# Kernel tuning notes

Measured on AMD Instinct MI355X. Metric: run time of the kernel, lower is better.

The kernel has to match this reference:

```python
import jax, jax.numpy as jnp
import numpy as np

T, R = 4, 6
HID, HEADS, LAYERS, OUT = 64, 8, 2, 4
DH = HID // HEADS
N = [100000, 200000, 20000, 2000]          # author, paper, term, conference
FEAT = [334, 512, 128, 128]
REL = [(0, 1), (1, 0), (1, 2), (2, 1), (1, 3), (3, 1)]   # (src_type, dst_type)
E = [800000, 800000, 1000000, 1000000, 200000, 200000]
NAMES = ['author', 'paper', 'term', 'conf']


def setup_inputs() -> dict:
    key = jax.random.key(0)
    ks = iter(jax.random.split(key, 64))
    inp = {}
    for t in range(T):
        inp[f'x_{NAMES[t]}'] = jax.random.normal(next(ks), (N[t], FEAT[t]), jnp.float32)
    for t in range(T):
        inp[f'W_in_{NAMES[t]}'] = jax.random.normal(next(ks), (FEAT[t], HID), jnp.float32) / np.sqrt(FEAT[t]).astype(np.float32)
        inp[f'b_in_{NAMES[t]}'] = jnp.zeros((HID,), jnp.float32)
    for nm in ['KW', 'QW', 'VW', 'AW']:
        inp[nm] = jax.random.normal(next(ks), (LAYERS, T, HID, HID), jnp.float32) / np.sqrt(HID).astype(np.float32)
    for nm in ['Kb', 'Qb', 'Vb', 'Ab']:
        inp[nm] = jnp.zeros((LAYERS, T, HID), jnp.float32)
    inp['skip'] = jnp.ones((LAYERS, T), jnp.float32)
    inp['A_rel'] = jax.random.normal(next(ks), (LAYERS, R, HEADS, DH, DH), jnp.float32) / np.sqrt(DH).astype(np.float32)
    inp['M_rel'] = jax.random.normal(next(ks), (LAYERS, R, HEADS, DH, DH), jnp.float32) / np.sqrt(DH).astype(np.float32)
    inp['P_rel'] = jnp.ones((LAYERS, R, HEADS), jnp.float32)
    inp['W_out'] = jax.random.normal(next(ks), (HID, OUT), jnp.float32) / np.sqrt(HID).astype(np.float32)
    inp['b_out'] = jnp.zeros((OUT,), jnp.float32)
    for r in range(R):
        s, d = REL[r]
        src = jax.random.randint(next(ks), (E[r],), 0, N[s], dtype=jnp.int32)
        dst = jax.random.randint(next(ks), (E[r],), 0, N[d], dtype=jnp.int32)
        inp[f'ei_{r}'] = jnp.stack([src, dst])
    return inp


def _segment_softmax(scores, seg, num):
    # scores: [E, HEADS]; softmax over edges sharing the same destination node
    m = jax.ops.segment_max(scores, seg, num_segments=num)
    ex = jnp.exp(scores - m[seg])
    den = jax.ops.segment_sum(ex, seg, num_segments=num)
    return ex / den[seg]


def _forward(xs, Wins, bins, KW, Kb, QW, Qb, VW, Vb, AW, Ab, skip,
             A_rel, M_rel, P_rel, W_out, b_out, eis):
    scale = np.float32(1.0 / np.sqrt(DH))
    h = [jax.nn.relu(x @ W + b) for x, W, b in zip(xs, Wins, bins)]
    for l in range(LAYERS):
        K = [(h[t] @ KW[l, t] + Kb[l, t]).reshape(-1, HEADS, DH) for t in range(T)]
        Q = [(h[t] @ QW[l, t] + Qb[l, t]).reshape(-1, HEADS, DH) for t in range(T)]
        V = [(h[t] @ VW[l, t] + Vb[l, t]).reshape(-1, HEADS, DH) for t in range(T)]
        out = [jnp.zeros((N[t], HID), h[t].dtype) for t in range(T)]
        for r in range(R):
            s, d = REL[r]
            src, dst = eis[r][0], eis[r][1]
            k = jnp.einsum('ehd,hdf->ehf', K[s][src], A_rel[l, r])   # [E,H,dh]
            v = jnp.einsum('ehd,hdf->ehf', V[s][src], M_rel[l, r])
            q = Q[d][dst]
            score = (q * k).sum(-1) * P_rel[l, r] * scale            # [E,H]
            alpha = _segment_softmax(score, dst, N[d])
            msg = (v * alpha[..., None]).reshape(-1, HID)
            out[d] = out[d] + jax.ops.segment_sum(msg, dst, num_segments=N[d])
        newh = []
        for t in range(T):
            o = jax.nn.gelu(out[t], approximate=False) @ AW[l, t] + Ab[l, t]
            g = jax.nn.sigmoid(skip[l, t])
            newh.append(g * o + (1.0 - g) * h[t])
        h = newh
    return h[0] @ W_out + b_out  # author logits


def reference(x_author, x_paper, x_term, x_conf,
              W_in_author, b_in_author, W_in_paper, b_in_paper,
              W_in_term, b_in_term, W_in_conf, b_in_conf,
              KW, Kb, QW, Qb, VW, Vb, AW, Ab, skip,
              A_rel, M_rel, P_rel, W_out, b_out,
              ei_0, ei_1, ei_2, ei_3, ei_4, ei_5):
    xs = [x_author, x_paper, x_term, x_conf]
    Wins = [W_in_author, W_in_paper, W_in_term, W_in_conf]
    bins = [b_in_author, b_in_paper, b_in_term, b_in_conf]
    eis = [ei_0, ei_1, ei_2, ei_3, ei_4, ei_5]
    return _forward(xs, Wins, bins, KW, Kb, QW, Qb, VW, Vb, AW, Ab, skip,
                    A_rel, M_rel, P_rel, W_out, b_out, eis)
```

## Files before the change

kernel.cpp:

```cpp
#include <hip/hip_runtime.h>
#include <math.h>

#define HID 64
#define HEADS 8
#define DH 8
#define TT 4
#define RR 6
#define LAYERS 2
#define NTOT 322000

static const int NS[TT]    = {100000, 200000, 20000, 2000};
static const int FEATS[TT] = {334, 512, 128, 128};
static const int RSRC[RR]  = {0, 1, 1, 2, 1, 3};
static const int RDST[RR]  = {1, 0, 2, 1, 3, 1};


__global__ void fill_f(float* __restrict__ p, float v, int n) {
    int i = blockIdx.x * 256 + threadIdx.x;
    if (i < n) p[i] = v;
}

__global__ void fill_i(int* __restrict__ p, int v, int n) {
    int i = blockIdx.x * 256 + threadIdx.x;
    if (i < n) p[i] = v;
}


__device__ __forceinline__ void load_x16(const float* __restrict__ xp, int F, int k0,
                                         bool f4ok, float xv[16]) {
    int rem = F - k0;
    if (xp && rem > 0) {
        if (rem >= 16) {
            if (f4ok) {
#pragma unroll
                for (int j = 0; j < 4; ++j) {
                    float4 v = *(const float4*)(xp + k0 + 4 * j);
                    xv[4 * j + 0] = v.x; xv[4 * j + 1] = v.y;
                    xv[4 * j + 2] = v.z; xv[4 * j + 3] = v.w;
                }
            } else {
#pragma unroll
                for (int j = 0; j < 8; ++j) {
                    float2 v = *(const float2*)(xp + k0 + 2 * j);
                    xv[2 * j + 0] = v.x; xv[2 * j + 1] = v.y;
                }
            }
        } else {
#pragma unroll
            for (int k = 0; k < 16; ++k) xv[k] = (k < rem) ? xp[k0 + k] : 0.f;
        }
    } else {
#pragma unroll
        for (int k = 0; k < 16; ++k) xv[k] = 0.f;
    }
}

__device__ __forceinline__ float4 load_w4(const float* __restrict__ W, int F,
                                          int f, int c) {
    float4 wv;
    if (f < F) wv = *(const float4*)(W + (size_t)f * 64 + c);
    else { wv.x = 0.f; wv.y = 0.f; wv.z = 0.f; wv.w = 0.f; }
    return wv;
}

template<int PREG, int POST>
__global__ __launch_bounds__(256) void gemm_n64(
    const float* __restrict__ X,
    const float* __restrict__ Wa, const float* __restrict__ Wb, const float* __restrict__ Wc,
    const float* __restrict__ ba, const float* __restrict__ bb, const float* __restrict__ bc,
    float* __restrict__ Ca, float* __restrict__ Cb, float* __restrict__ Cc,
    const float* __restrict__ skipv, int lt,
    int Nrows, int F)
{
    const float* W = Wa; const float* bias = ba; float* C = Ca;
    if (blockIdx.y == 1) { W = Wb; bias = bb; C = Cb; }
    else if (blockIdx.y == 2) { W = Wc; bias = bc; C = Cc; }

    __shared__ float xs[16][256];
    __shared__ float ws[16][64];

    int tid = threadIdx.x;
    int row0 = blockIdx.x * 256;
    int myrow = row0 + tid;
    const float* xp = (myrow < Nrows) ? (X + (size_t)myrow * F) : (const float*)0;

    int cg = tid & 7;
    int rs = tid >> 3;
    int xoff = rs * 8;
    int woff = cg * 8;

    int wi_f = tid >> 4;
    int wi_c = (tid & 15) * 4;

    float acc[8][8];
#pragma unroll
    for (int i = 0; i < 8; ++i)
#pragma unroll
        for (int j = 0; j < 8; ++j) acc[i][j] = 0.f;

    const bool f4ok = ((F & 3) == 0);

    float xv[16];
    float4 wv;
    load_x16(xp, F, 0, f4ok, xv);
    wv = load_w4(W, F, wi_f, wi_c);

    for (int k0 = 0; k0 < F; k0 += 16) {
        __syncthreads();
        if (PREG) {
#pragma unroll
            for (int k = 0; k < 16; ++k) {
                float v = xv[k];
                xs[k][tid] = 0.5f * v * (1.f + erff(v * 0.7071067811865475f));
            }
        } else {
#pragma unroll
            for (int k = 0; k < 16; ++k) xs[k][tid] = xv[k];
        }
        *(float4*)&ws[wi_f][wi_c] = wv;
        __syncthreads();

        if (k0 + 16 < F) {
            load_x16(xp, F, k0 + 16, f4ok, xv);
            wv = load_w4(W, F, k0 + 16 + wi_f, wi_c);
        }

#pragma unroll
        for (int k = 0; k < 16; ++k) {
            float xr[8], wr[8];
#pragma unroll
            for (int j = 0; j < 8; ++j) xr[j] = xs[k][xoff + j];
#pragma unroll
            for (int j = 0; j < 8; ++j) wr[j] = ws[k][woff + j];
#pragma unroll
            for (int i = 0; i < 8; ++i)
#pragma unroll
                for (int j = 0; j < 8; ++j)
                    acc[i][j] = fmaf(xr[i], wr[j], acc[i][j]);
        }
    }

    float bv[8];
#pragma unroll
    for (int j = 0; j < 8; ++j) bv[j] = bias[woff + j];
    float g = 1.f, invg = 0.f;
    if (POST == 2) {
        float s = skipv[lt];
        g = 1.f / (1.f + __expf(-s));
        invg = 1.f - g;
    }
#pragma unroll
    for (int i = 0; i < 8; ++i) {
        int r = row0 + xoff + i;
        if (r < Nrows) {
            size_t base = (size_t)r * 64 + woff;
            float o[8];
#pragma unroll
            for (int j = 0; j < 8; ++j) o[j] = acc[i][j] + bv[j];
            if (POST == 1) {
#pragma unroll
                for (int j = 0; j < 8; ++j) o[j] = fmaxf(o[j], 0.f);
            }
            if (POST == 2) {
#pragma unroll
                for (int j = 0; j < 8; ++j) o[j] = g * o[j] + invg * C[base + j];
            }
            float4 s0, s1;
            s0.x = o[0]; s0.y = o[1]; s0.z = o[2]; s0.w = o[3];
            s1.x = o[4]; s1.y = o[5]; s1.z = o[6]; s1.w = o[7];
            *(float4*)(C + base)     = s0;
            *(float4*)(C + base + 4) = s1;
        }
    }
}

__global__ void out_proj(const float* __restrict__ h, const float* __restrict__ W,
                         const float* __restrict__ b, float* __restrict__ out, int n4) {
    int idx = blockIdx.x * 256 + threadIdx.x;
    if (idx >= n4) return;
    int row = idx >> 2, c = idx & 3;
    float acc = b[c];
    const float* hp = h + (size_t)row * 64;
    for (int f = 0; f < 64; ++f) acc = fmaf(hp[f], W[f * 4 + c], acc);
    out[idx] = acc;
}


__global__ void hist_k(const int* __restrict__ dst, int* __restrict__ deg, int E) {
    int i = blockIdx.x * 256 + threadIdx.x;
    if (i < E) atomicAdd(&deg[dst[i]], 1);
}

__global__ void scan1(const int* __restrict__ deg, int* __restrict__ bsum, int n) {
    __shared__ int sdata[256];
    int tid = threadIdx.x;
    int base = blockIdx.x * 1024 + tid * 4;
    int s = 0;
#pragma unroll
    for (int j = 0; j < 4; ++j) if (base + j < n) s += deg[base + j];
    sdata[tid] = s;
    __syncthreads();
    for (int off = 128; off > 0; off >>= 1) {
        if (tid < off) sdata[tid] += sdata[tid + off];
        __syncthreads();
    }
    if (tid == 0) bsum[blockIdx.x] = sdata[0];
}

__global__ void scan2(int* __restrict__ bsum, int nb) {
    if (blockIdx.x == 0 && threadIdx.x == 0) {
        int run = 0;
        for (int i = 0; i < nb; ++i) { int t = bsum[i]; bsum[i] = run; run += t; }
    }
}

__global__ void scan3(const int* __restrict__ deg, const int* __restrict__ bsum,
                      int* __restrict__ rp, int n, int E) {
    __shared__ int sc[256];
    int tid = threadIdx.x;
    int base = blockIdx.x * 1024 + tid * 4;
    int v0 = 0, v1 = 0, v2 = 0, v3 = 0;
    if (base + 0 < n) v0 = deg[base + 0];
    if (base + 1 < n) v1 = deg[base + 1];
    if (base + 2 < n) v2 = deg[base + 2];
    if (base + 3 < n) v3 = deg[base + 3];
    int s = v0 + v1 + v2 + v3;
    sc[tid] = s;
    __syncthreads();
    for (int off = 1; off < 256; off <<= 1) {
        int t = (tid >= off) ? sc[tid - off] : 0;
        __syncthreads();
        sc[tid] += t;
        __syncthreads();
    }
    int run = bsum[blockIdx.x] + sc[tid] - s;
    if (base + 0 < n) { rp[base + 0] = run; run += v0; }
    if (base + 1 < n) { rp[base + 1] = run; run += v1; }
    if (base + 2 < n) { rp[base + 2] = run; run += v2; }
    if (base + 3 < n) { rp[base + 3] = run; run += v3; }
    if (blockIdx.x == 0 && tid == 0) rp[n] = E;
}

__global__ void scatter_k(const int* __restrict__ src, const int* __restrict__ dst,
                          const int* __restrict__ rp, int* __restrict__ cnt,
                          int* __restrict__ col, int E) {
    int i = blockIdx.x * 256 + threadIdx.x;
    if (i >= E) return;
    int d = dst[i];
    int p = rp[d] + atomicAdd(&cnt[d], 1);
    col[p] = src[i];
}

__global__ __launch_bounds__(256) void rel_attn(
    const int* __restrict__ row_ptr, const int* __restrict__ col,
    const float* __restrict__ K, const float* __restrict__ Q, const float* __restrict__ V,
    const float* __restrict__ A, const float* __restrict__ M, const float* __restrict__ P,
    float* __restrict__ outb, int Nd)
{
    __shared__ float As[512], Ms[512], Ps[8];
    int tid = threadIdx.x;
    for (int i = tid; i < 512; i += 256) { As[i] = A[i]; Ms[i] = M[i]; }
    if (tid < 8) Ps[tid] = P[tid];
    __syncthreads();
    int wave = tid >> 6, lane = tid & 63;
    int d = blockIdx.x * 4 + wave;
    if (d >= Nd) return;
    int hh = lane >> 3, ff = lane & 7;
    int gbase = lane & 56;

    float q = Q[(size_t)d * 64 + lane];
    float qhat = 0.f;
#pragma unroll
    for (int f = 0; f < 8; ++f)
        qhat = fmaf(__shfl(q, gbase + f, 64), As[hh * 64 + ff * 8 + f], qhat);
    qhat *= Ps[hh] * 0.35355339059327373f;

    int e0 = row_ptr[d], e1 = row_ptr[d + 1];
    float m = -INFINITY, lsum = 0.f, acc = 0.f;
    for (int e = e0; e < e1; ++e) {
        int s = col[e];
        float kv = K[(size_t)s * 64 + lane];
        float vv = V[(size_t)s * 64 + lane];
        float p = kv * qhat;
        p += __shfl_xor(p, 1, 64);
        p += __shfl_xor(p, 2, 64);
        p += __shfl_xor(p, 4, 64);
        float mn = fmaxf(m, p);
        float aa = __expf(m - mn);
        float w  = __expf(p - mn);
        lsum = lsum * aa + w;
        acc  = acc * aa + w * vv;
        m = mn;
    }
    float o = 0.f;
#pragma unroll
    for (int dd = 0; dd < 8; ++dd)
        o = fmaf(__shfl(acc, gbase + dd, 64), Ms[hh * 64 + dd * 8 + ff], o);
    float inv = (lsum > 0.f) ? 1.f / lsum : 0.f;
    outb[(size_t)d * 64 + lane] += o * inv;
}


extern "C" void kernel_launch(void* const* d_in, const int* in_sizes, int n_in,
                              void* d_out, int out_size, void* d_ws, size_t ws_size,
                              hipStream_t stream) {
    const float* x[TT]    = {(const float*)d_in[0], (const float*)d_in[1],
                             (const float*)d_in[2], (const float*)d_in[3]};
    const float* Win[TT]  = {(const float*)d_in[4], (const float*)d_in[6],
                             (const float*)d_in[8], (const float*)d_in[10]};
    const float* bin[TT]  = {(const float*)d_in[5], (const float*)d_in[7],
                             (const float*)d_in[9], (const float*)d_in[11]};
    const float* KW = (const float*)d_in[12];
    const float* QW = (const float*)d_in[13];
    const float* VW = (const float*)d_in[14];
    const float* AW = (const float*)d_in[15];
    const float* Kb = (const float*)d_in[16];
    const float* Qb = (const float*)d_in[17];
    const float* Vb = (const float*)d_in[18];
    const float* Ab = (const float*)d_in[19];
    const float* skip  = (const float*)d_in[20];
    const float* A_rel = (const float*)d_in[21];
    const float* M_rel = (const float*)d_in[22];
    const float* P_rel = (const float*)d_in[23];
    const float* W_out = (const float*)d_in[24];
    const float* b_out = (const float*)d_in[25];
    const int* ei[RR] = {(const int*)d_in[26], (const int*)d_in[27], (const int*)d_in[28],
                         (const int*)d_in[29], (const int*)d_in[30], (const int*)d_in[31]};
    int E[RR];
    for (int r = 0; r < RR; ++r) E[r] = in_sizes[26 + r] / 2;

    float* ws = (float*)d_ws;
    size_t off = 0;
    float* h    = ws + off; off += (size_t)NTOT * 64;
    float* K    = ws + off; off += (size_t)NTOT * 64;
    float* Q    = ws + off; off += (size_t)NTOT * 64;
    float* V    = ws + off; off += (size_t)NTOT * 64;
    float* outb = ws + off; off += (size_t)NTOT * 64;
    int* ibase = (int*)(ws + off);
    size_t ioff = 0;
    int* col_all = ibase + ioff;
    int colOff[RR]; int acc_e = 0;
    for (int r = 0; r < RR; ++r) { colOff[r] = acc_e; acc_e += E[r]; }
    ioff += (size_t)acc_e;
    int* rp_all = ibase + ioff;
    int rpOff[RR]; int acc_rp = 0;
    for (int r = 0; r < RR; ++r) { rpOff[r] = acc_rp; acc_rp += NS[RDST[r]] + 1; }
    ioff += (size_t)acc_rp;
    int* deg  = ibase + ioff; ioff += 200000;
    int* cnt  = ibase + ioff; ioff += 200000;
    int* bsum = ibase + ioff; ioff += 256;

    int nodeOff[TT] = {0, 100000, 300000, 320000};

    for (int r = 0; r < RR; ++r) {
        int Nd = NS[RDST[r]];
        const int* srcIdx = ei[r];
        const int* dstIdx = ei[r] + E[r];
        int* rp  = rp_all + rpOff[r];
        int* col = col_all + colOff[r];
        fill_i<<<(Nd + 255) / 256, 256, 0, stream>>>(deg, 0, Nd);
        fill_i<<<(Nd + 255) / 256, 256, 0, stream>>>(cnt, 0, Nd);
        hist_k<<<(E[r] + 255) / 256, 256, 0, stream>>>(dstIdx, deg, E[r]);
        int nb = (Nd + 1023) / 1024;
        scan1<<<nb, 256, 0, stream>>>(deg, bsum, Nd);
        scan2<<<1, 64, 0, stream>>>(bsum, nb);
        scan3<<<nb, 256, 0, stream>>>(deg, bsum, rp, Nd, E[r]);
        scatter_k<<<(E[r] + 255) / 256, 256, 0, stream>>>(srcIdx, dstIdx, rp, cnt, col, E[r]);
    }

    for (int t = 0; t < TT; ++t) {
        dim3 grid((NS[t] + 255) / 256, 1);
        gemm_n64<0, 1><<<grid, 256, 0, stream>>>(
            x[t], Win[t], Win[t], Win[t], bin[t], bin[t], bin[t],
            h + (size_t)nodeOff[t] * 64, h + (size_t)nodeOff[t] * 64, h + (size_t)nodeOff[t] * 64,
            (const float*)0, 0, NS[t], FEATS[t]);
    }

    for (int l = 0; l < LAYERS; ++l) {
        for (int t = 0; t < TT; ++t) {
            size_t wOff = (size_t)(l * TT + t) * 64 * 64;
            size_t bOff = (size_t)(l * TT + t) * 64;
            size_t nOff = (size_t)nodeOff[t] * 64;
            dim3 grid((NS[t] + 255) / 256, 3);
            gemm_n64<0, 0><<<grid, 256, 0, stream>>>(
                h + nOff, KW + wOff, QW + wOff, VW + wOff,
                Kb + bOff, Qb + bOff, Vb + bOff,
                K + nOff, Q + nOff, V + nOff,
                (const float*)0, 0, NS[t], 64);
        }
        fill_f<<<((size_t)NTOT * 64 + 255) / 256, 256, 0, stream>>>(outb, 0.f, NTOT * 64);

        for (int r = 0; r < RR; ++r) {
            int s = RSRC[r], d = RDST[r];
            int Nd = NS[d];
            const float* Ar = A_rel + (size_t)(l * RR + r) * HEADS * 64;
            const float* Mr = M_rel + (size_t)(l * RR + r) * HEADS * 64;
            const float* Pr = P_rel + (size_t)(l * RR + r) * HEADS;
            rel_attn<<<(Nd + 3) / 4, 256, 0, stream>>>(
                rp_all + rpOff[r], col_all + colOff[r],
                K + (size_t)nodeOff[s] * 64, Q + (size_t)nodeOff[d] * 64,
                V + (size_t)nodeOff[s] * 64, Ar, Mr, Pr,
                outb + (size_t)nodeOff[d] * 64, Nd);
        }

        for (int t = 0; t < TT; ++t) {
            size_t wOff = (size_t)(l * TT + t) * 64 * 64;
            size_t bOff = (size_t)(l * TT + t) * 64;
            size_t nOff = (size_t)nodeOff[t] * 64;
            dim3 grid((NS[t] + 255) / 256, 1);
            gemm_n64<1, 2><<<grid, 256, 0, stream>>>(
                outb + nOff, AW + wOff, AW + wOff, AW + wOff,
                Ab + bOff, Ab + bOff, Ab + bOff,
                h + nOff, h + nOff, h + nOff,
                skip, l * TT + t, NS[t], 64);
        }
    }

    out_proj<<<(NS[0] * 4 + 255) / 256, 256, 0, stream>>>(h, W_out, b_out,
                                                          (float*)d_out, NS[0] * 4);
}
```

Measured before the change: 3.784 ms.

## Merge per-relation attention launches into one grid with atomic output and prefetched gathers

Replaces the six per-relation rel_attn launches with a single kernel. Each block looks up its relation in a block-offset table, and relations sharing a destination type add into the output with atomics. The edge loop is also unrolled by four, and the next group's K/V rows are prefetched into registers to overlap the gather latency. The goal is to cut launch gaps and tail underutilisation and to hide gather latency. The cost is float atomics, which make the summation order nondeterministic, plus extra register pressure.

```diff
diff --git a/kernel.cpp b/kernel.cpp
--- a/kernel.cpp
+++ b/kernel.cpp
@@ -251,24 +251,51 @@
     col[p] = src[i];
 }
 
-__global__ __launch_bounds__(256) void rel_attn(
-    const int* __restrict__ row_ptr, const int* __restrict__ col,
+
+struct RelTab {
+    int blockStart[RR + 1];
+    int rpOff[RR];
+    int colOff[RR];
+    int srcOff[RR];
+    int dstOff[RR];
+    int nd[RR];
+};
+
+__global__ __launch_bounds__(256) void rel_attn_all(
+    const int* __restrict__ rp_all, const int* __restrict__ col_all,
     const float* __restrict__ K, const float* __restrict__ Q, const float* __restrict__ V,
-    const float* __restrict__ A, const float* __restrict__ M, const float* __restrict__ P,
-    float* __restrict__ outb, int Nd)
+    const float* __restrict__ Abase, const float* __restrict__ Mbase,
+    const float* __restrict__ Pbase,
+    float* __restrict__ outb, RelTab tab)
 {
+    int bx = blockIdx.x;
+    int r = 0;
+#pragma unroll
+    for (int i = 1; i < RR; ++i) if (bx >= tab.blockStart[i]) r = i;
+
     __shared__ float As[512], Ms[512], Ps[8];
     int tid = threadIdx.x;
+    const float* A = Abase + (size_t)r * 512;
+    const float* M = Mbase + (size_t)r * 512;
+    const float* P = Pbase + (size_t)r * 8;
     for (int i = tid; i < 512; i += 256) { As[i] = A[i]; Ms[i] = M[i]; }
     if (tid < 8) Ps[tid] = P[tid];
     __syncthreads();
+
     int wave = tid >> 6, lane = tid & 63;
-    int d = blockIdx.x * 4 + wave;
-    if (d >= Nd) return;
-    int hh = lane >> 3, ff = lane & 7;
-    int gbase = lane & 56;
-
-    float q = Q[(size_t)d * 64 + lane];
+    int d = (bx - tab.blockStart[r]) * 4 + wave;
+    if (d >= tab.nd[r]) return;
+
+    const int* row_ptr = rp_all + tab.rpOff[r];
+    const int* col     = col_all + tab.colOff[r];
+    const float* Ks = K + (size_t)tab.srcOff[r] * 64;
+    const float* Vs = V + (size_t)tab.srcOff[r] * 64;
+    const float* Qd = Q + (size_t)tab.dstOff[r] * 64;
+    float* outd = outb + (size_t)tab.dstOff[r] * 64;
+
+    int hh = lane >> 3, ff = lane & 7, gbase = lane & 56;
+
+    float q = Qd[(size_t)d * 64 + lane];
     float qhat = 0.f;
 #pragma unroll
     for (int f = 0; f < 8; ++f)
@@ -277,27 +304,81 @@
 
     int e0 = row_ptr[d], e1 = row_ptr[d + 1];
     float m = -INFINITY, lsum = 0.f, acc = 0.f;
-    for (int e = e0; e < e1; ++e) {
+
+    int e = e0;
+    int eend4 = e0 + ((e1 - e0) & ~3);
+
+    if (e < eend4) {
+        float ka[4], va[4];
+        {
+            int sa[4];
+#pragma unroll
+            for (int j = 0; j < 4; ++j) sa[j] = col[e + j];
+#pragma unroll
+            for (int j = 0; j < 4; ++j) {
+                ka[j] = Ks[(size_t)sa[j] * 64 + lane];
+                va[j] = Vs[(size_t)sa[j] * 64 + lane];
+            }
+        }
+        while (true) {
+            int en = e + 4;
+            bool more = (en < eend4);
+            float kb[4], vb[4];
+            if (more) {
+                int sb[4];
+#pragma unroll
+                for (int j = 0; j < 4; ++j) sb[j] = col[en + j];
+#pragma unroll
+                for (int j = 0; j < 4; ++j) {
+                    kb[j] = Ks[(size_t)sb[j] * 64 + lane];
+                    vb[j] = Vs[(size_t)sb[j] * 64 + lane];
+                }
+            }
+            float p[4];
+#pragma unroll
+            for (int j = 0; j < 4; ++j) {
+                float t = ka[j] * qhat;
+                t += __shfl_xor(t, 1, 64);
+                t += __shfl_xor(t, 2, 64);
+                t += __shfl_xor(t, 4, 64);
+                p[j] = t;
+            }
+            float mn = fmaxf(m, fmaxf(fmaxf(p[0], p[1]), fmaxf(p[2], p[3])));
+            float aa = __expf(m - mn);
+            float w0 = __expf(p[0] - mn), w1 = __expf(p[1] - mn);
+            float w2 = __expf(p[2] - mn), w3 = __expf(p[3] - mn);
+            lsum = lsum * aa + ((w0 + w1) + (w2 + w3));
+            acc  = fmaf(acc, aa,
+                   fmaf(w0, va[0], fmaf(w1, va[1], fmaf(w2, va[2], w3 * va[3]))));
+            m = mn;
+            e = en;
+            if (!more) break;
+#pragma unroll
+            for (int j = 0; j < 4; ++j) { ka[j] = kb[j]; va[j] = vb[j]; }
+        }
+    }
+    for (; e < e1; ++e) {
         int s = col[e];
-        float kv = K[(size_t)s * 64 + lane];
-        float vv = V[(size_t)s * 64 + lane];
-        float p = kv * qhat;
-        p += __shfl_xor(p, 1, 64);
-        p += __shfl_xor(p, 2, 64);
-        p += __shfl_xor(p, 4, 64);
-        float mn = fmaxf(m, p);
+        float kv = Ks[(size_t)s * 64 + lane];
+        float vv = Vs[(size_t)s * 64 + lane];
+        float t = kv * qhat;
+        t += __shfl_xor(t, 1, 64);
+        t += __shfl_xor(t, 2, 64);
+        t += __shfl_xor(t, 4, 64);
+        float mn = fmaxf(m, t);
         float aa = __expf(m - mn);
-        float w  = __expf(p - mn);
+        float w  = __expf(t - mn);
         lsum = lsum * aa + w;
         acc  = acc * aa + w * vv;
         m = mn;
     }
+
     float o = 0.f;
 #pragma unroll
     for (int dd = 0; dd < 8; ++dd)
         o = fmaf(__shfl(acc, gbase + dd, 64), Ms[hh * 64 + dd * 8 + ff], o);
     float inv = (lsum > 0.f) ? 1.f / lsum : 0.f;
-    outb[(size_t)d * 64 + lane] += o * inv;
+    atomicAdd(&outd[(size_t)d * 64 + lane], o * inv);
 }
 
 
@@ -368,6 +449,19 @@
         scatter_k<<<(E[r] + 255) / 256, 256, 0, stream>>>(srcIdx, dstIdx, rp, cnt, col, E[r]);
     }
 
+    RelTab tab;
+    int bacc = 0;
+    for (int r = 0; r < RR; ++r) {
+        tab.blockStart[r] = bacc;
+        bacc += (NS[RDST[r]] + 3) / 4;
+        tab.rpOff[r]  = rpOff[r];
+        tab.colOff[r] = colOff[r];
+        tab.srcOff[r] = nodeOff[RSRC[r]];
+        tab.dstOff[r] = nodeOff[RDST[r]];
+        tab.nd[r]     = NS[RDST[r]];
+    }
+    tab.blockStart[RR] = bacc;
+
     for (int t = 0; t < TT; ++t) {
         dim3 grid((NS[t] + 255) / 256, 1);
         gemm_n64<0, 1><<<grid, 256, 0, stream>>>(
@@ -390,18 +484,12 @@
         }
         fill_f<<<((size_t)NTOT * 64 + 255) / 256, 256, 0, stream>>>(outb, 0.f, NTOT * 64);
 
-        for (int r = 0; r < RR; ++r) {
-            int s = RSRC[r], d = RDST[r];
-            int Nd = NS[d];
-            const float* Ar = A_rel + (size_t)(l * RR + r) * HEADS * 64;
-            const float* Mr = M_rel + (size_t)(l * RR + r) * HEADS * 64;
-            const float* Pr = P_rel + (size_t)(l * RR + r) * HEADS;
-            rel_attn<<<(Nd + 3) / 4, 256, 0, stream>>>(
-                rp_all + rpOff[r], col_all + colOff[r],
-                K + (size_t)nodeOff[s] * 64, Q + (size_t)nodeOff[d] * 64,
-                V + (size_t)nodeOff[s] * 64, Ar, Mr, Pr,
-                outb + (size_t)nodeOff[d] * 64, Nd);
-        }
+        rel_attn_all<<<bacc, 256, 0, stream>>>(
+            rp_all, col_all, K, Q, V,
+            A_rel + (size_t)l * RR * 512,
+            M_rel + (size_t)l * RR * 512,
+            P_rel + (size_t)l * RR * 8,
+            outb, tab);
 
         for (int t = 0; t < TT; ++t) {
             size_t wOff = (size_t)(l * TT + t) * 64 * 64;
```

New measurement: 3.176 ms. -16.1%, faster.
